# Kernel optimization log

Hardware: AMD Instinct MI355X
Metric: run time of the kernel (lower is better)

## Reference

```python
import jax, jax.numpy as jnp
import numpy as np

S = 4  # spixel_downsize


def _shift2d(x, oy, ox):
    # out[..., y, x] = x[..., y - oy, x - ox] if in-bounds else 0 (zero pad)
    pad = [(0, 0)] * (x.ndim - 2) + [(S, S), (S, S)]
    xp = jnp.pad(x, pad)
    h, w = x.shape[-2], x.shape[-1]
    return xp[..., S - oy:S - oy + h, S - ox:S - ox + w]


def _valid_mask(h, w, oy, ox):
    ys = jnp.arange(h)
    xs = jnp.arange(w)
    my = (ys - oy >= 0) & (ys - oy < h)
    mx = (xs - ox >= 0) & (xs - ox < w)
    return my[:, None] & mx[None, :]


def _conv3d(x, w, stride, pad):
    return jax.lax.conv_general_dilated(
        x, w, window_strides=stride, padding=[(p, p) for p in pad],
        dimension_numbers=('NCDHW', 'OIDHW', 'NCDHW'))


def _basic(x, w, stride, pad):
    # BasicConv: Conv3d(bias=False) + BN(identity at init) + ReLU
    return jax.nn.relu(_conv3d(x, w, stride, pad))


def setup_inputs() -> dict:
    key = jax.random.key(0)
    ks = jax.random.split(key, 8)
    cv = jax.random.normal(ks[0], (1, 8, 24, 128, 256), jnp.float32)
    sp = jax.random.uniform(ks[1], (1, 9, 128, 256), jnp.float32)
    xy = jax.random.normal(ks[2], (1, 2, 128, 256), jnp.float32)
    w_stem = jax.random.normal(ks[3], (16, 72, 1, 1, 1), jnp.float32) * 0.05
    w1a = jax.random.normal(ks[4], (32, 16, 3, 2, 2), jnp.float32) * 0.05
    w1b = jax.random.normal(ks[5], (32, 32, 3, 1, 1), jnp.float32) * 0.05
    w2a = jax.random.normal(ks[6], (64, 32, 3, 2, 2), jnp.float32) * 0.05
    w2b = jax.random.normal(ks[7], (64, 64, 3, 1, 1), jnp.float32) * 0.05
    return dict(cv=cv, sp=sp, xy=xy, w_stem=w_stem, w1a=w1a, w1b=w1b, w2a=w2a, w2b=w2b)


def reference(cv, sp, xy, w_stem, w1a, w1b, w2a, w2b):
    b, c, d, h, w = cv.shape
    feats, probs = [], []
    uv0 = jnp.zeros((b, 2, h, w), cv.dtype)
    # 9 shifted neighbors; neighbor k shifts by (S*((k//3)-1), S*((k%3)-1)).
    # All uv writes in the original target slot 0 and sequentially overwrite;
    for k in range(9):
        oy = S * ((k // 3) - 1)
        ox = S * ((k % 3) - 1)
        p = _shift2d(sp[:, k], oy, ox)                      # (b,h,w), zeros outside
        probs.append(p)
        feats.append(_shift2d(cv, oy, ox) * p[:, None, None])  # (b,c,d,h,w)
        u = _shift2d(xy, oy, ox) * p[:, None]               # (b,2,h,w)
        mask = _valid_mask(h, w, oy, ox)[None, None]
        uv0 = jnp.where(mask, u, uv0)
    # (b, c, 9, d, h, w) -> (b, 9c, d, h, w), matching torch reshape order
    feat = jnp.stack(feats, axis=2).reshape(b, c * 9, d, h, w)
    prob_sum = jnp.sum(jnp.stack(probs, axis=1), axis=1, keepdims=True)  # (b,1,h,w)
    tot = prob_sum.reshape(b, 1, h // S, S, w // S, S).mean((3, 5))      # avg_pool2d
    tot_up = jnp.repeat(jnp.repeat(tot, S, axis=2), S, axis=3)           # nearest upsample
    feat = feat / tot_up[:, :, None]                                     # (b,9c,d,h,w)
    feat = _basic(feat, w_stem, (1, 1, 1), (0, 0, 0))
    f1 = _basic(feat, w1a, (2, 2, 2), (1, 0, 0))
    f1 = _basic(f1, w1b, (1, 1, 1), (1, 0, 0))
    f2 = _basic(f1, w2a, (2, 2, 2), (1, 0, 0))
    f2 = _basic(f2, w2b, (1, 1, 1), (1, 0, 0))
    # uv.sum(2) == uv0 since only neighbor-slot 0 is written
    uv = uv0.reshape(b, 2, h // S, S, w // S, S).mean((3, 5)) / tot      # (b,2,h/S,w/S)
    return f1, f2, uv.reshape(b, 2, -1)
```

## Files before the change

### kernel.cpp

```cpp
#include <hip/hip_runtime.h>

#define HH 128
#define WW 256
#define HW (HH * WW)

#define OFF_TOT   0
#define OFF_WT    2048
#define WT_STEM   0
#define WT_1A     1152
#define WT_1B     7296
#define WT_2A     10368
#define WT_2B     34944
#define OFF_STEM  49280
#define OFF_F1A   12632192
#define OFF_F1N   15777920
#define OFF_F2A   49280

__global__ __launch_bounds__(256) void k_pre(
    const float* __restrict__ sp, const float* __restrict__ xy,
    const float* __restrict__ wstem, const float* __restrict__ w1a,
    const float* __restrict__ w1b, const float* __restrict__ w2a,
    const float* __restrict__ w2b,
    float* __restrict__ tot, float* __restrict__ uv_out, float* __restrict__ wt)
{
  int gid = blockIdx.x * 256 + threadIdx.x;
  if (gid < 1152) { int o = gid & 15, r = gid >> 4; int ci = r / 9, k = r - ci * 9;
    wt[WT_STEM + gid] = wstem[o * 72 + ci * 9 + k]; }
  if (gid < 6144) { int o = gid & 31, ci = (gid >> 5) & 15, tp = gid >> 9;
    wt[WT_1A + gid] = w1a[o * 192 + ci * 12 + tp]; }
  if (gid < 3072) { int o = gid & 31, ci = (gid >> 5) & 31, kd = gid >> 10;
    wt[WT_1B + gid] = w1b[(o * 32 + ci) * 3 + kd]; }
  if (gid < 24576) { int o = gid & 63, ci = (gid >> 6) & 31, tp = gid >> 11;
    wt[WT_2A + gid] = w2a[o * 384 + ci * 12 + tp]; }
  if (gid < 12288) { int o = gid & 63, ci = (gid >> 6) & 63, kd = gid >> 12;
    wt[WT_2B + gid] = w2b[(o * 64 + ci) * 3 + kd]; }
  if (gid < 8192) {
    int cell = gid >> 2, q = gid & 3;
    int Y = cell >> 6, X = cell & 63;
    float tsum = 0.f, u0 = 0.f, u1 = 0.f;
    int y = Y * 4 + q;
#pragma unroll
    for (int j = 0; j < 4; ++j) {
      int x = X * 4 + j;
      float psum = 0.f;
#pragma unroll
      for (int k = 0; k < 9; ++k) {
        int oy = 4 * ((k / 3) - 1), ox = 4 * ((k % 3) - 1);
        int sy = y - oy, sx = x - ox;
        if (sy >= 0 && sy < HH && sx >= 0 && sx < WW)
          psum += sp[k * HW + sy * WW + sx];
      }
      tsum += psum;
      int oy = (y >= 4) ? 4 : 0;
      int ox = (x >= 4) ? 4 : 0;
      int kk = (oy ? 2 : 1) * 3 + (ox ? 2 : 1);
      int sy = y - oy, sx = x - ox;
      float p = sp[kk * HW + sy * WW + sx];
      u0 += xy[sy * WW + sx] * p;
      u1 += xy[HW + sy * WW + sx] * p;
    }
    tsum += __shfl_xor(tsum, 1); tsum += __shfl_xor(tsum, 2);
    u0 += __shfl_xor(u0, 1); u0 += __shfl_xor(u0, 2);
    u1 += __shfl_xor(u1, 1); u1 += __shfl_xor(u1, 2);
    if (q == 0) {
      float t = tsum * (1.f / 16.f);
      tot[cell] = t;
      float inv = 1.f / t;
      uv_out[cell] = u0 * (1.f / 16.f) * inv;
      uv_out[2048 + cell] = u1 * (1.f / 16.f) * inv;
    }
  }
}

__global__ __launch_bounds__(256) void k_stem(
    const float* __restrict__ cv, const float* __restrict__ sp,
    const float* __restrict__ wt, const float* __restrict__ tot,
    float* __restrict__ out)
{
  __shared__ float wl[1152];
  for (int i = threadIdx.x; i < 1152; i += 256) wl[i] = wt[i];
  __syncthreads();
  int x0 = blockIdx.x * 128 + 2 * (threadIdx.x & 63);
  int y  = blockIdx.y * 4 + (threadIdx.x >> 6);
  int d  = blockIdx.z;
  float2 p2[9]; int off[9];
#pragma unroll
  for (int k = 0; k < 9; ++k) {
    int oy = 4 * ((k / 3) - 1), ox = 4 * ((k % 3) - 1);
    int sy = y - oy, sx = x0 - ox;
    bool v = (sy >= 0) && (sy < HH) && (sx >= 0) && (sx < WW - 1);
    int syc = v ? sy : 0, sxc = v ? sx : 0;
    off[k] = syc * WW + sxc;
    float2 t = *(const float2*)(sp + k * HW + off[k]);
    p2[k].x = v ? t.x : 0.f;
    p2[k].y = v ? t.y : 0.f;
  }
  float acc[16][2];
#pragma unroll
  for (int o = 0; o < 16; ++o) { acc[o][0] = 0.f; acc[o][1] = 0.f; }
  const float* cvd = cv + (size_t)d * HW;
  float2 cb[2][9];
#pragma unroll
  for (int k = 0; k < 9; ++k) cb[0][k] = *(const float2*)(cvd + off[k]);
#pragma unroll
  for (int ci = 0; ci < 8; ++ci) {
    if (ci < 7) {
#pragma unroll
      for (int k = 0; k < 9; ++k)
        cb[(ci + 1) & 1][k] = *(const float2*)(cvd + (size_t)(ci + 1) * 24 * HW + off[k]);
    }
#pragma unroll
    for (int k = 0; k < 9; ++k) {
      float t0 = cb[ci & 1][k].x * p2[k].x;
      float t1 = cb[ci & 1][k].y * p2[k].y;
      const float* wb = &wl[(ci * 9 + k) * 16];
      float wv[16];
#pragma unroll
      for (int q = 0; q < 4; ++q) *(float4*)&wv[q * 4] = *(const float4*)(wb + q * 4);
#pragma unroll
      for (int o = 0; o < 16; ++o) {
        acc[o][0] += wv[o] * t0;
        acc[o][1] += wv[o] * t1;
      }
    }
  }
  float inv = 1.f / tot[(y >> 2) * 64 + (x0 >> 2)];
  float* op = out + (((size_t)d * HH + y) * WW + x0) * 16;
#pragma unroll
  for (int p = 0; p < 2; ++p)
#pragma unroll
    for (int q = 0; q < 4; ++q) {
      float4 v;
      v.x = fmaxf(acc[q * 4 + 0][p] * inv, 0.f);
      v.y = fmaxf(acc[q * 4 + 1][p] * inv, 0.f);
      v.z = fmaxf(acc[q * 4 + 2][p] * inv, 0.f);
      v.w = fmaxf(acc[q * 4 + 3][p] * inv, 0.f);
      *(float4*)(op + p * 16 + q * 4) = v;
    }
}

__global__ __launch_bounds__(256) void k_conv1a(
    const float* __restrict__ in, const float* __restrict__ wt,
    float* __restrict__ out)
{
  __shared__ float wl[1536];
  int og = blockIdx.z;
  for (int i = threadIdx.x; i < 1536; i += 256) {
    int o = i & 7, ci = (i >> 3) & 15, tap = i >> 7;
    wl[i] = wt[tap * 512 + ci * 32 + og * 8 + o];
  }
  __syncthreads();
  int xo = threadIdx.x & 127;
  int yo = blockIdx.x * 2 + (threadIdx.x >> 7);
  int dz = blockIdx.y;
  float acc[8];
#pragma unroll
  for (int o = 0; o < 8; ++o) acc[o] = 0.f;
  float ib[2][32];
  {
    int dd = 2 * dz - 1; dd = dd < 0 ? 0 : dd;
    const float4* ip = (const float4*)(in + (((size_t)dd * 128 + 2 * yo) * 256 + 2 * xo) * 16);
#pragma unroll
    for (int q = 0; q < 8; ++q) {
      float4 t = ip[q];
      ib[0][q * 4] = t.x; ib[0][q * 4 + 1] = t.y; ib[0][q * 4 + 2] = t.z; ib[0][q * 4 + 3] = t.w;
    }
  }
#pragma unroll
  for (int w = 0; w < 6; ++w) {
    if (w < 5) {
      int kd = (w + 1) >> 1, ky = (w + 1) & 1;
      int dd = 2 * dz - 1 + kd; dd = dd < 0 ? 0 : dd;
      int y = 2 * yo + ky;
      const float4* ip = (const float4*)(in + (((size_t)dd * 128 + y) * 256 + 2 * xo) * 16);
#pragma unroll
      for (int q = 0; q < 8; ++q) {
        float4 t = ip[q];
        ib[(w + 1) & 1][q * 4] = t.x; ib[(w + 1) & 1][q * 4 + 1] = t.y;
        ib[(w + 1) & 1][q * 4 + 2] = t.z; ib[(w + 1) & 1][q * 4 + 3] = t.w;
      }
    }
    if (2 * dz - 1 + (w >> 1) >= 0) {
#pragma unroll
      for (int kx = 0; kx < 2; ++kx) {
        const float* wsl = &wl[(w * 2 + kx) * 128];
#pragma unroll
        for (int ci = 0; ci < 16; ++ci) {
          float wv[8];
          *(float4*)&wv[0] = *(const float4*)(wsl + ci * 8);
          *(float4*)&wv[4] = *(const float4*)(wsl + ci * 8 + 4);
          float a = ib[w & 1][kx * 16 + ci];
#pragma unroll
          for (int o = 0; o < 8; ++o) acc[o] += wv[o] * a;
        }
      }
    }
  }
  float* op = out + (((size_t)dz * 64 + yo) * 128 + xo) * 32 + og * 8;
  float4 v0, v1;
  v0.x = fmaxf(acc[0], 0.f); v0.y = fmaxf(acc[1], 0.f);
  v0.z = fmaxf(acc[2], 0.f); v0.w = fmaxf(acc[3], 0.f);
  v1.x = fmaxf(acc[4], 0.f); v1.y = fmaxf(acc[5], 0.f);
  v1.z = fmaxf(acc[6], 0.f); v1.w = fmaxf(acc[7], 0.f);
  *(float4*)op = v0; *(float4*)(op + 4) = v1;
}

__global__ __launch_bounds__(256) void k_conv1b(
    const float* __restrict__ in, const float* __restrict__ wt,
    float* __restrict__ outn, float* __restrict__ outc)
{
  __shared__ float wl[768];
  int og = blockIdx.z;
  for (int i = threadIdx.x; i < 768; i += 256) {
    int o = i & 7, ci = (i >> 3) & 31, kd = i >> 8;
    wl[i] = wt[kd * 1024 + ci * 32 + og * 8 + o];
  }
  __syncthreads();
  int xo = threadIdx.x & 127;
  int yo = blockIdx.x * 2 + (threadIdx.x >> 7);
  int dz = blockIdx.y;
  float acc[8];
#pragma unroll
  for (int o = 0; o < 8; ++o) acc[o] = 0.f;
  float ib[2][32];
  {
    int dd = dz - 1; dd = dd < 0 ? 0 : dd;
    const float4* ip = (const float4*)(in + (((size_t)dd * 64 + yo) * 128 + xo) * 32);
#pragma unroll
    for (int q = 0; q < 8; ++q) {
      float4 t = ip[q];
      ib[0][q * 4] = t.x; ib[0][q * 4 + 1] = t.y; ib[0][q * 4 + 2] = t.z; ib[0][q * 4 + 3] = t.w;
    }
  }
#pragma unroll
  for (int w = 0; w < 3; ++w) {
    if (w < 2) {
      int dd = dz + w;  dd = dd >= 12 ? 11 : dd;
      const float4* ip = (const float4*)(in + (((size_t)dd * 64 + yo) * 128 + xo) * 32);
#pragma unroll
      for (int q = 0; q < 8; ++q) {
        float4 t = ip[q];
        ib[(w + 1) & 1][q * 4] = t.x; ib[(w + 1) & 1][q * 4 + 1] = t.y;
        ib[(w + 1) & 1][q * 4 + 2] = t.z; ib[(w + 1) & 1][q * 4 + 3] = t.w;
      }
    }
    int d_ = dz - 1 + w;
    if (d_ >= 0 && d_ < 12) {
      const float* wsl = &wl[w * 256];
#pragma unroll
      for (int ci = 0; ci < 32; ++ci) {
        float wv[8];
        *(float4*)&wv[0] = *(const float4*)(wsl + ci * 8);
        *(float4*)&wv[4] = *(const float4*)(wsl + ci * 8 + 4);
        float a = ib[w & 1][ci];
#pragma unroll
        for (int o = 0; o < 8; ++o) acc[o] += wv[o] * a;
      }
    }
  }
  float* onp = outn + (((size_t)dz * 64 + yo) * 128 + xo) * 32 + og * 8;
  float4 v0, v1;
  v0.x = fmaxf(acc[0], 0.f); v0.y = fmaxf(acc[1], 0.f);
  v0.z = fmaxf(acc[2], 0.f); v0.w = fmaxf(acc[3], 0.f);
  v1.x = fmaxf(acc[4], 0.f); v1.y = fmaxf(acc[5], 0.f);
  v1.z = fmaxf(acc[6], 0.f); v1.w = fmaxf(acc[7], 0.f);
  *(float4*)onp = v0; *(float4*)(onp + 4) = v1;
#pragma unroll
  for (int o = 0; o < 8; ++o)
    outc[((size_t)((og * 8 + o) * 12 + dz) * 64 + yo) * 128 + xo] = fmaxf(acc[o], 0.f);
}

__global__ __launch_bounds__(256) void k_conv2a(
    const float* __restrict__ in, const float* __restrict__ wt,
    float* __restrict__ out)
{
  __shared__ float wl[1536];
  int og = blockIdx.z;
  for (int i = threadIdx.x; i < 1536; i += 256) {
    int o = i & 3, ci = (i >> 2) & 31, tap = i >> 7;
    wl[i] = wt[tap * 2048 + ci * 64 + og * 4 + o];
  }
  __syncthreads();
  int xo = threadIdx.x & 63;
  int yo = blockIdx.x * 4 + (threadIdx.x >> 6);
  int dz = blockIdx.y;
  float acc[4] = {0.f, 0.f, 0.f, 0.f};
  float ib[2][32];
  {
    int dd = 2 * dz - 1; dd = dd < 0 ? 0 : dd;
    const float4* ip = (const float4*)(in + (((size_t)dd * 64 + 2 * yo) * 128 + 2 * xo) * 32);
#pragma unroll
    for (int q = 0; q < 8; ++q) {
      float4 t = ip[q];
      ib[0][q * 4] = t.x; ib[0][q * 4 + 1] = t.y; ib[0][q * 4 + 2] = t.z; ib[0][q * 4 + 3] = t.w;
    }
  }
#pragma unroll
  for (int w = 0; w < 12; ++w) {
    if (w < 11) {
      int wn = w + 1;
      int kd = wn >> 2, ky = (wn >> 1) & 1, kx = wn & 1;
      int dd = 2 * dz - 1 + kd; dd = dd < 0 ? 0 : dd;
      int y = 2 * yo + ky, x = 2 * xo + kx;
      const float4* ip = (const float4*)(in + (((size_t)dd * 64 + y) * 128 + x) * 32);
#pragma unroll
      for (int q = 0; q < 8; ++q) {
        float4 t = ip[q];
        ib[wn & 1][q * 4] = t.x; ib[wn & 1][q * 4 + 1] = t.y;
        ib[wn & 1][q * 4 + 2] = t.z; ib[wn & 1][q * 4 + 3] = t.w;
      }
    }
    if (2 * dz - 1 + (w >> 2) >= 0) {
      const float* wsl = &wl[w * 128];
#pragma unroll
      for (int ci = 0; ci < 32; ++ci) {
        float wv[4];
        *(float4*)&wv[0] = *(const float4*)(wsl + ci * 4);
        float a = ib[w & 1][ci];
#pragma unroll
        for (int o = 0; o < 4; ++o) acc[o] += wv[o] * a;
      }
    }
  }
  float4 v;
  v.x = fmaxf(acc[0], 0.f); v.y = fmaxf(acc[1], 0.f);
  v.z = fmaxf(acc[2], 0.f); v.w = fmaxf(acc[3], 0.f);
  *(float4*)(out + (((size_t)dz * 32 + yo) * 64 + xo) * 64 + og * 4) = v;
}

__global__ __launch_bounds__(256) void k_conv2b(
    const float* __restrict__ in, const float* __restrict__ wt,
    float* __restrict__ out)
{
  __shared__ float wl[768];
  int og = blockIdx.z;
  for (int i = threadIdx.x; i < 768; i += 256) {
    int o = i & 3, ci = (i >> 2) & 63, kd = i >> 8;
    wl[i] = wt[kd * 4096 + ci * 64 + og * 4 + o];
  }
  __syncthreads();
  int xo = threadIdx.x & 63;
  int yo = blockIdx.x * 4 + (threadIdx.x >> 6);
  int dz = blockIdx.y;
  float acc[4] = {0.f, 0.f, 0.f, 0.f};
  float ib[2][32];
  {
    int dd = dz - 1; dd = dd < 0 ? 0 : dd;
    const float4* ip = (const float4*)(in + (((size_t)dd * 32 + yo) * 64 + xo) * 64);
#pragma unroll
    for (int q = 0; q < 8; ++q) {
      float4 t = ip[q];
      ib[0][q * 4] = t.x; ib[0][q * 4 + 1] = t.y; ib[0][q * 4 + 2] = t.z; ib[0][q * 4 + 3] = t.w;
    }
  }
#pragma unroll
  for (int w = 0; w < 6; ++w) {
    if (w < 5) {
      int wn = w + 1;
      int kd = wn >> 1, hf = wn & 1;
      int dd = dz - 1 + kd; dd = dd < 0 ? 0 : (dd >= 6 ? 5 : dd);
      const float4* ip = (const float4*)(in + (((size_t)dd * 32 + yo) * 64 + xo) * 64 + hf * 32);
#pragma unroll
      for (int q = 0; q < 8; ++q) {
        float4 t = ip[q];
        ib[wn & 1][q * 4] = t.x; ib[wn & 1][q * 4 + 1] = t.y;
        ib[wn & 1][q * 4 + 2] = t.z; ib[wn & 1][q * 4 + 3] = t.w;
      }
    }
    int d_ = dz - 1 + (w >> 1);
    if (d_ >= 0 && d_ < 6) {
      const float* wsl = &wl[w * 128];
#pragma unroll
      for (int ci = 0; ci < 32; ++ci) {
        float wv[4];
        *(float4*)&wv[0] = *(const float4*)(wsl + ci * 4);
        float a = ib[w & 1][ci];
#pragma unroll
        for (int o = 0; o < 4; ++o) acc[o] += wv[o] * a;
      }
    }
  }
#pragma unroll
  for (int o = 0; o < 4; ++o)
    out[((size_t)((og * 4 + o) * 6 + dz) * 32 + yo) * 64 + xo] = fmaxf(acc[o], 0.f);
}

extern "C" void kernel_launch(void* const* d_in, const int* in_sizes, int n_in,
                              void* d_out, int out_size, void* d_ws, size_t ws_size,
                              hipStream_t stream) {
  const float* cv    = (const float*)d_in[0];
  const float* sp    = (const float*)d_in[1];
  const float* xy    = (const float*)d_in[2];
  const float* wstem = (const float*)d_in[3];
  const float* w1a   = (const float*)d_in[4];
  const float* w1b   = (const float*)d_in[5];
  const float* w2a   = (const float*)d_in[6];
  const float* w2b   = (const float*)d_in[7];
  float* out = (float*)d_out;
  float* out_f1 = out;
  float* out_f2 = out + 3145728;
  float* out_uv = out + 3145728 + 786432;

  float* ws = (float*)d_ws;
  float* t_tot  = ws + OFF_TOT;
  float* wt     = ws + OFF_WT;
  float* t_stem = ws + OFF_STEM;
  float* t_f1a  = ws + OFF_F1A;
  float* t_f1n  = ws + OFF_F1N;
  float* t_f2a  = ws + OFF_F2A;

  k_pre<<<96, 256, 0, stream>>>(sp, xy, wstem, w1a, w1b, w2a, w2b,
                                t_tot, out_uv, wt);
  k_stem<<<dim3(2, 32, 24), 256, 0, stream>>>(cv, sp, wt + WT_STEM, t_tot, t_stem);
  k_conv1a<<<dim3(32, 12, 4), 256, 0, stream>>>(t_stem, wt + WT_1A, t_f1a);
  k_conv1b<<<dim3(32, 12, 4), 256, 0, stream>>>(t_f1a, wt + WT_1B, t_f1n, out_f1);
  k_conv2a<<<dim3(8, 6, 16), 256, 0, stream>>>(t_f1n, wt + WT_2A, t_f2a);
  k_conv2b<<<dim3(8, 6, 16), 256, 0, stream>>>(t_f2a, wt + WT_2B, out_f2);
}
```

Before: 181.6 us.

## Register-block conv kernels over 4 output pixels and use packed fp32 FMA

Each conv kernel (stem, conv1a, conv1b) now computes four adjacent output pixels per thread and splits output channels across blocks, so weights read from shared memory are reused across more pixels. Inner loops use two-wide vector FMA (v2f) so the compiler can emit packed fp32 FMA instructions. The input channel loop is chunked to keep register use bounded. In exchange, per-thread loads become strided across pixels, register pressure rises, and the stem now reads cv once per channel group, i.e. twice in total.

```diff
diff --git a/kernel.cpp b/kernel.cpp
--- a/kernel.cpp
+++ b/kernel.cpp
@@ -3,6 +3,16 @@
 #define HH 128
 #define WW 256
 #define HW (HH * WW)
+
+typedef float v2f __attribute__((ext_vector_type(2)));
+
+static __device__ __forceinline__ v2f fma2(v2f a, v2f b, v2f c) {
+#if __has_builtin(__builtin_elementwise_fma)
+  return __builtin_elementwise_fma(a, b, c);
+#else
+  return a * b + c;
+#endif
+}
 
 #define OFF_TOT   0
 #define OFF_WT    2048
@@ -77,66 +87,75 @@
     const float* __restrict__ wt, const float* __restrict__ tot,
     float* __restrict__ out)
 {
-  __shared__ float wl[1152];
-  for (int i = threadIdx.x; i < 1152; i += 256) wl[i] = wt[i];
+  __shared__ float wl[576];
+  int og = blockIdx.x;
+  for (int i = threadIdx.x; i < 576; i += 256)
+    wl[i] = wt[(i >> 3) * 16 + og * 8 + (i & 7)];
   __syncthreads();
-  int x0 = blockIdx.x * 128 + 2 * (threadIdx.x & 63);
+  int x0 = 4 * (threadIdx.x & 63);
   int y  = blockIdx.y * 4 + (threadIdx.x >> 6);
   int d  = blockIdx.z;
-  float2 p2[9]; int off[9];
+  int off[9];
+  float4 p4[9];
 #pragma unroll
   for (int k = 0; k < 9; ++k) {
     int oy = 4 * ((k / 3) - 1), ox = 4 * ((k % 3) - 1);
     int sy = y - oy, sx = x0 - ox;
-    bool v = (sy >= 0) && (sy < HH) && (sx >= 0) && (sx < WW - 1);
+    bool v = (sy >= 0) && (sy < HH) && (sx >= 0) && (sx <= WW - 4);
     int syc = v ? sy : 0, sxc = v ? sx : 0;
     off[k] = syc * WW + sxc;
-    float2 t = *(const float2*)(sp + k * HW + off[k]);
-    p2[k].x = v ? t.x : 0.f;
-    p2[k].y = v ? t.y : 0.f;
-  }
-  float acc[16][2];
-#pragma unroll
-  for (int o = 0; o < 16; ++o) { acc[o][0] = 0.f; acc[o][1] = 0.f; }
+    float4 t = *(const float4*)(sp + k * HW + off[k]);
+    float4 z = {0.f, 0.f, 0.f, 0.f};
+    p4[k] = v ? t : z;
+  }
+  v2f acc[4][4];
+#pragma unroll
+  for (int a = 0; a < 4; ++a)
+#pragma unroll
+    for (int p = 0; p < 4; ++p) acc[a][p] = (v2f){0.f, 0.f};
   const float* cvd = cv + (size_t)d * HW;
-  float2 cb[2][9];
-#pragma unroll
-  for (int k = 0; k < 9; ++k) cb[0][k] = *(const float2*)(cvd + off[k]);
+  float4 c[2];
+  c[0] = *(const float4*)(cvd + off[0]);
 #pragma unroll
   for (int ci = 0; ci < 8; ++ci) {
-    if (ci < 7) {
-#pragma unroll
-      for (int k = 0; k < 9; ++k)
-        cb[(ci + 1) & 1][k] = *(const float2*)(cvd + (size_t)(ci + 1) * 24 * HW + off[k]);
-    }
 #pragma unroll
     for (int k = 0; k < 9; ++k) {
-      float t0 = cb[ci & 1][k].x * p2[k].x;
-      float t1 = cb[ci & 1][k].y * p2[k].y;
-      const float* wb = &wl[(ci * 9 + k) * 16];
-      float wv[16];
-#pragma unroll
-      for (int q = 0; q < 4; ++q) *(float4*)&wv[q * 4] = *(const float4*)(wb + q * 4);
-#pragma unroll
-      for (int o = 0; o < 16; ++o) {
-        acc[o][0] += wv[o] * t0;
-        acc[o][1] += wv[o] * t1;
-      }
+      int n = ci * 9 + k;
+      if (n < 71) {
+        int n1 = n + 1, ci1 = n1 / 9, k1 = n1 - ci1 * 9;
+        c[n1 & 1] = *(const float4*)(cvd + (size_t)ci1 * 24 * HW + off[k1]);
+      }
+      float4 cc = c[n & 1];
+      float4 pp = p4[k];
+      float t0 = cc.x * pp.x, t1 = cc.y * pp.y, t2 = cc.z * pp.z, t3 = cc.w * pp.w;
+      const float* wb = &wl[n * 8];
+      float4 wq0 = *(const float4*)wb;
+      float4 wq1 = *(const float4*)(wb + 4);
+      v2f w0 = {wq0.x, wq0.y}, w1 = {wq0.z, wq0.w};
+      v2f w2 = {wq1.x, wq1.y}, w3 = {wq1.z, wq1.w};
+      v2f s0 = {t0, t0}, s1 = {t1, t1}, s2 = {t2, t2}, s3 = {t3, t3};
+      acc[0][0] = fma2(w0, s0, acc[0][0]); acc[1][0] = fma2(w1, s0, acc[1][0]);
+      acc[2][0] = fma2(w2, s0, acc[2][0]); acc[3][0] = fma2(w3, s0, acc[3][0]);
+      acc[0][1] = fma2(w0, s1, acc[0][1]); acc[1][1] = fma2(w1, s1, acc[1][1]);
+      acc[2][1] = fma2(w2, s1, acc[2][1]); acc[3][1] = fma2(w3, s1, acc[3][1]);
+      acc[0][2] = fma2(w0, s2, acc[0][2]); acc[1][2] = fma2(w1, s2, acc[1][2]);
+      acc[2][2] = fma2(w2, s2, acc[2][2]); acc[3][2] = fma2(w3, s2, acc[3][2]);
+      acc[0][3] = fma2(w0, s3, acc[0][3]); acc[1][3] = fma2(w1, s3, acc[1][3]);
+      acc[2][3] = fma2(w2, s3, acc[2][3]); acc[3][3] = fma2(w3, s3, acc[3][3]);
     }
   }
   float inv = 1.f / tot[(y >> 2) * 64 + (x0 >> 2)];
-  float* op = out + (((size_t)d * HH + y) * WW + x0) * 16;
-#pragma unroll
-  for (int p = 0; p < 2; ++p)
-#pragma unroll
-    for (int q = 0; q < 4; ++q) {
-      float4 v;
-      v.x = fmaxf(acc[q * 4 + 0][p] * inv, 0.f);
-      v.y = fmaxf(acc[q * 4 + 1][p] * inv, 0.f);
-      v.z = fmaxf(acc[q * 4 + 2][p] * inv, 0.f);
-      v.w = fmaxf(acc[q * 4 + 3][p] * inv, 0.f);
-      *(float4*)(op + p * 16 + q * 4) = v;
-    }
+  float* op = out + (((size_t)d * HH + y) * WW + x0) * 16 + og * 8;
+#pragma unroll
+  for (int p = 0; p < 4; ++p) {
+    float4 v0, v1;
+    v0.x = fmaxf(acc[0][p].x * inv, 0.f); v0.y = fmaxf(acc[0][p].y * inv, 0.f);
+    v0.z = fmaxf(acc[1][p].x * inv, 0.f); v0.w = fmaxf(acc[1][p].y * inv, 0.f);
+    v1.x = fmaxf(acc[2][p].x * inv, 0.f); v1.y = fmaxf(acc[2][p].y * inv, 0.f);
+    v1.z = fmaxf(acc[3][p].x * inv, 0.f); v1.w = fmaxf(acc[3][p].y * inv, 0.f);
+    *(float4*)(op + p * 16) = v0;
+    *(float4*)(op + p * 16 + 4) = v1;
+  }
 }
 
 __global__ __launch_bounds__(256) void k_conv1a(
@@ -150,124 +169,164 @@
     wl[i] = wt[tap * 512 + ci * 32 + og * 8 + o];
   }
   __syncthreads();
-  int xo = threadIdx.x & 127;
-  int yo = blockIdx.x * 2 + (threadIdx.x >> 7);
+  int xq = threadIdx.x & 31;
+  int xo0 = 4 * xq;
+  int yo = blockIdx.x * 8 + (threadIdx.x >> 5);
   int dz = blockIdx.y;
-  float acc[8];
-#pragma unroll
-  for (int o = 0; o < 8; ++o) acc[o] = 0.f;
+  v2f acc[4][4];
+#pragma unroll
+  for (int a = 0; a < 4; ++a)
+#pragma unroll
+    for (int p = 0; p < 4; ++p) acc[a][p] = (v2f){0.f, 0.f};
   float ib[2][32];
   {
     int dd = 2 * dz - 1; dd = dd < 0 ? 0 : dd;
-    const float4* ip = (const float4*)(in + (((size_t)dd * 128 + 2 * yo) * 256 + 2 * xo) * 16);
-#pragma unroll
-    for (int q = 0; q < 8; ++q) {
-      float4 t = ip[q];
-      ib[0][q * 4] = t.x; ib[0][q * 4 + 1] = t.y; ib[0][q * 4 + 2] = t.z; ib[0][q * 4 + 3] = t.w;
-    }
-  }
-#pragma unroll
-  for (int w = 0; w < 6; ++w) {
-    if (w < 5) {
-      int kd = (w + 1) >> 1, ky = (w + 1) & 1;
-      int dd = 2 * dz - 1 + kd; dd = dd < 0 ? 0 : dd;
-      int y = 2 * yo + ky;
-      const float4* ip = (const float4*)(in + (((size_t)dd * 128 + y) * 256 + 2 * xo) * 16);
-#pragma unroll
-      for (int q = 0; q < 8; ++q) {
-        float4 t = ip[q];
-        ib[(w + 1) & 1][q * 4] = t.x; ib[(w + 1) & 1][q * 4 + 1] = t.y;
-        ib[(w + 1) & 1][q * 4 + 2] = t.z; ib[(w + 1) & 1][q * 4 + 3] = t.w;
-      }
-    }
-    if (2 * dz - 1 + (w >> 1) >= 0) {
+    const float* base = in + (((size_t)dd * 128 + 2 * yo) * 256 + 8 * xq) * 16;
+#pragma unroll
+    for (int i = 0; i < 8; ++i) {
+      float4 t = *(const float4*)(base + i * 16);
+      ib[0][i * 4] = t.x; ib[0][i * 4 + 1] = t.y; ib[0][i * 4 + 2] = t.z; ib[0][i * 4 + 3] = t.w;
+    }
+  }
+#pragma unroll
+  for (int m = 0; m < 24; ++m) {
+    int kd = m >> 3, ky = (m >> 2) & 1, c4 = m & 3;
+    if (m < 23) {
+      int mn = m + 1;
+      int nkd = mn >> 3, nky = (mn >> 2) & 1, nc4 = mn & 3;
+      int dd = 2 * dz - 1 + nkd; dd = dd < 0 ? 0 : dd;
+      int y = 2 * yo + nky;
+      const float* base = in + (((size_t)dd * 128 + y) * 256 + 8 * xq) * 16 + nc4 * 4;
+#pragma unroll
+      for (int i = 0; i < 8; ++i) {
+        float4 t = *(const float4*)(base + i * 16);
+        ib[mn & 1][i * 4] = t.x; ib[mn & 1][i * 4 + 1] = t.y;
+        ib[mn & 1][i * 4 + 2] = t.z; ib[mn & 1][i * 4 + 3] = t.w;
+      }
+    }
+    if (2 * dz - 1 + kd >= 0) {
 #pragma unroll
       for (int kx = 0; kx < 2; ++kx) {
-        const float* wsl = &wl[(w * 2 + kx) * 128];
-#pragma unroll
-        for (int ci = 0; ci < 16; ++ci) {
-          float wv[8];
-          *(float4*)&wv[0] = *(const float4*)(wsl + ci * 8);
-          *(float4*)&wv[4] = *(const float4*)(wsl + ci * 8 + 4);
-          float a = ib[w & 1][kx * 16 + ci];
-#pragma unroll
-          for (int o = 0; o < 8; ++o) acc[o] += wv[o] * a;
+        int tap = (kd * 2 + ky) * 2 + kx;
+#pragma unroll
+        for (int j = 0; j < 4; ++j) {
+          int ci = c4 * 4 + j;
+          const float* wb = &wl[tap * 128 + ci * 8];
+          float4 wq0 = *(const float4*)wb;
+          float4 wq1 = *(const float4*)(wb + 4);
+          v2f w0 = {wq0.x, wq0.y}, w1 = {wq0.z, wq0.w};
+          v2f w2 = {wq1.x, wq1.y}, w3 = {wq1.z, wq1.w};
+#pragma unroll
+          for (int px = 0; px < 4; ++px) {
+            float a = ib[m & 1][(2 * px + kx) * 4 + j];
+            v2f as = {a, a};
+            acc[0][px] = fma2(w0, as, acc[0][px]);
+            acc[1][px] = fma2(w1, as, acc[1][px]);
+            acc[2][px] = fma2(w2, as, acc[2][px]);
+            acc[3][px] = fma2(w3, as, acc[3][px]);
+          }
         }
       }
     }
   }
-  float* op = out + (((size_t)dz * 64 + yo) * 128 + xo) * 32 + og * 8;
-  float4 v0, v1;
-  v0.x = fmaxf(acc[0], 0.f); v0.y = fmaxf(acc[1], 0.f);
-  v0.z = fmaxf(acc[2], 0.f); v0.w = fmaxf(acc[3], 0.f);
-  v1.x = fmaxf(acc[4], 0.f); v1.y = fmaxf(acc[5], 0.f);
-  v1.z = fmaxf(acc[6], 0.f); v1.w = fmaxf(acc[7], 0.f);
-  *(float4*)op = v0; *(float4*)(op + 4) = v1;
+  float* op = out + (((size_t)dz * 64 + yo) * 128 + xo0) * 32 + og * 8;
+#pragma unroll
+  for (int px = 0; px < 4; ++px) {
+    float4 v0, v1;
+    v0.x = fmaxf(acc[0][px].x, 0.f); v0.y = fmaxf(acc[0][px].y, 0.f);
+    v0.z = fmaxf(acc[1][px].x, 0.f); v0.w = fmaxf(acc[1][px].y, 0.f);
+    v1.x = fmaxf(acc[2][px].x, 0.f); v1.y = fmaxf(acc[2][px].y, 0.f);
+    v1.z = fmaxf(acc[3][px].x, 0.f); v1.w = fmaxf(acc[3][px].y, 0.f);
+    *(float4*)(op + px * 32) = v0;
+    *(float4*)(op + px * 32 + 4) = v1;
+  }
 }
 
 __global__ __launch_bounds__(256) void k_conv1b(
     const float* __restrict__ in, const float* __restrict__ wt,
     float* __restrict__ outn, float* __restrict__ outc)
 {
-  __shared__ float wl[768];
+  __shared__ float wl[384];
   int og = blockIdx.z;
-  for (int i = threadIdx.x; i < 768; i += 256) {
-    int o = i & 7, ci = (i >> 3) & 31, kd = i >> 8;
-    wl[i] = wt[kd * 1024 + ci * 32 + og * 8 + o];
+  for (int i = threadIdx.x; i < 384; i += 256) {
+    int o = i & 3, ci = (i >> 2) & 31, kd = i >> 7;
+    wl[i] = wt[kd * 1024 + ci * 32 + og * 4 + o];
   }
   __syncthreads();
-  int xo = threadIdx.x & 127;
-  int yo = blockIdx.x * 2 + (threadIdx.x >> 7);
+  int xq = threadIdx.x & 31;
+  int xo0 = 4 * xq;
+  int yo = blockIdx.x * 8 + (threadIdx.x >> 5);
   int dz = blockIdx.y;
-  float acc[8];
-#pragma unroll
-  for (int o = 0; o < 8; ++o) acc[o] = 0.f;
+  v2f acc[2][4];
+#pragma unroll
+  for (int a = 0; a < 2; ++a)
+#pragma unroll
+    for (int p = 0; p < 4; ++p) acc[a][p] = (v2f){0.f, 0.f};
   float ib[2][32];
   {
     int dd = dz - 1; dd = dd < 0 ? 0 : dd;
-    const float4* ip = (const float4*)(in + (((size_t)dd * 64 + yo) * 128 + xo) * 32);
-#pragma unroll
-    for (int q = 0; q < 8; ++q) {
-      float4 t = ip[q];
-      ib[0][q * 4] = t.x; ib[0][q * 4 + 1] = t.y; ib[0][q * 4 + 2] = t.z; ib[0][q * 4 + 3] = t.w;
-    }
-  }
-#pragma unroll
-  for (int w = 0; w < 3; ++w) {
-    if (w < 2) {
-      int dd = dz + w;  dd = dd >= 12 ? 11 : dd;
-      const float4* ip = (const float4*)(in + (((size_t)dd * 64 + yo) * 128 + xo) * 32);
-#pragma unroll
-      for (int q = 0; q < 8; ++q) {
-        float4 t = ip[q];
-        ib[(w + 1) & 1][q * 4] = t.x; ib[(w + 1) & 1][q * 4 + 1] = t.y;
-        ib[(w + 1) & 1][q * 4 + 2] = t.z; ib[(w + 1) & 1][q * 4 + 3] = t.w;
-      }
-    }
-    int d_ = dz - 1 + w;
+    const float* base = in + (((size_t)dd * 64 + yo) * 128 + xo0) * 32;
+#pragma unroll
+    for (int i = 0; i < 4; ++i) {
+      float4 t0 = *(const float4*)(base + i * 32);
+      float4 t1 = *(const float4*)(base + i * 32 + 4);
+      ib[0][i * 8] = t0.x; ib[0][i * 8 + 1] = t0.y; ib[0][i * 8 + 2] = t0.z; ib[0][i * 8 + 3] = t0.w;
+      ib[0][i * 8 + 4] = t1.x; ib[0][i * 8 + 5] = t1.y; ib[0][i * 8 + 6] = t1.z; ib[0][i * 8 + 7] = t1.w;
+    }
+  }
+#pragma unroll
+  for (int m = 0; m < 12; ++m) {
+    int kd = m >> 2, ch = m & 3;
+    if (m < 11) {
+      int mn = m + 1;
+      int nkd = mn >> 2, nch = mn & 3;
+      int dd = dz - 1 + nkd; dd = dd < 0 ? 0 : (dd >= 12 ? 11 : dd);
+      const float* base = in + (((size_t)dd * 64 + yo) * 128 + xo0) * 32 + nch * 8;
+#pragma unroll
+      for (int i = 0; i < 4; ++i) {
+        float4 t0 = *(const float4*)(base + i * 32);
+        float4 t1 = *(const float4*)(base + i * 32 + 4);
+        ib[mn & 1][i * 8] = t0.x; ib[mn & 1][i * 8 + 1] = t0.y;
+        ib[mn & 1][i * 8 + 2] = t0.z; ib[mn & 1][i * 8 + 3] = t0.w;
+        ib[mn & 1][i * 8 + 4] = t1.x; ib[mn & 1][i * 8 + 5] = t1.y;
+        ib[mn & 1][i * 8 + 6] = t1.z; ib[mn & 1][i * 8 + 7] = t1.w;
+      }
+    }
+    int d_ = dz - 1 + kd;
     if (d_ >= 0 && d_ < 12) {
-      const float* wsl = &wl[w * 256];
-#pragma unroll
-      for (int ci = 0; ci < 32; ++ci) {
-        float wv[8];
-        *(float4*)&wv[0] = *(const float4*)(wsl + ci * 8);
-        *(float4*)&wv[4] = *(const float4*)(wsl + ci * 8 + 4);
-        float a = ib[w & 1][ci];
-#pragma unroll
-        for (int o = 0; o < 8; ++o) acc[o] += wv[o] * a;
-      }
-    }
-  }
-  float* onp = outn + (((size_t)dz * 64 + yo) * 128 + xo) * 32 + og * 8;
-  float4 v0, v1;
-  v0.x = fmaxf(acc[0], 0.f); v0.y = fmaxf(acc[1], 0.f);
-  v0.z = fmaxf(acc[2], 0.f); v0.w = fmaxf(acc[3], 0.f);
-  v1.x = fmaxf(acc[4], 0.f); v1.y = fmaxf(acc[5], 0.f);
-  v1.z = fmaxf(acc[6], 0.f); v1.w = fmaxf(acc[7], 0.f);
-  *(float4*)onp = v0; *(float4*)(onp + 4) = v1;
-#pragma unroll
-  for (int o = 0; o < 8; ++o)
-    outc[((size_t)((og * 8 + o) * 12 + dz) * 64 + yo) * 128 + xo] = fmaxf(acc[o], 0.f);
+#pragma unroll
+      for (int j = 0; j < 8; ++j) {
+        int ci = ch * 8 + j;
+        float4 wq = *(const float4*)&wl[kd * 128 + ci * 4];
+        v2f w0 = {wq.x, wq.y}, w1 = {wq.z, wq.w};
+#pragma unroll
+        for (int px = 0; px < 4; ++px) {
+          float a = ib[m & 1][px * 8 + j];
+          v2f as = {a, a};
+          acc[0][px] = fma2(w0, as, acc[0][px]);
+          acc[1][px] = fma2(w1, as, acc[1][px]);
+        }
+      }
+    }
+  }
+  float* onp = outn + (((size_t)dz * 64 + yo) * 128 + xo0) * 32 + og * 4;
+#pragma unroll
+  for (int px = 0; px < 4; ++px) {
+    float4 v;
+    v.x = fmaxf(acc[0][px].x, 0.f); v.y = fmaxf(acc[0][px].y, 0.f);
+    v.z = fmaxf(acc[1][px].x, 0.f); v.w = fmaxf(acc[1][px].y, 0.f);
+    *(float4*)(onp + px * 32) = v;
+  }
+#pragma unroll
+  for (int o = 0; o < 4; ++o) {
+    float4 v;
+    float a0 = (o & 1) ? acc[o >> 1][0].y : acc[o >> 1][0].x;
+    float a1 = (o & 1) ? acc[o >> 1][1].y : acc[o >> 1][1].x;
+    float a2 = (o & 1) ? acc[o >> 1][2].y : acc[o >> 1][2].x;
+    float a3 = (o & 1) ? acc[o >> 1][3].y : acc[o >> 1][3].x;
+    v.x = fmaxf(a0, 0.f); v.y = fmaxf(a1, 0.f); v.z = fmaxf(a2, 0.f); v.w = fmaxf(a3, 0.f);
+    *(float4*)(outc + (((size_t)(og * 4 + o) * 12 + dz) * 64 + yo) * 128 + xo0) = v;
+  }
 }
 
 __global__ __launch_bounds__(256) void k_conv2a(
@@ -284,7 +343,7 @@
   int xo = threadIdx.x & 63;
   int yo = blockIdx.x * 4 + (threadIdx.x >> 6);
   int dz = blockIdx.y;
-  float acc[4] = {0.f, 0.f, 0.f, 0.f};
+  v2f acc[2] = {{0.f, 0.f}, {0.f, 0.f}};
   float ib[2][32];
   {
     int dd = 2 * dz - 1; dd = dd < 0 ? 0 : dd;
@@ -314,17 +373,18 @@
       const float* wsl = &wl[w * 128];
 #pragma unroll
       for (int ci = 0; ci < 32; ++ci) {
-        float wv[4];
-        *(float4*)&wv[0] = *(const float4*)(wsl + ci * 4);
+        float4 wq = *(const float4*)(wsl + ci * 4);
+        v2f w0 = {wq.x, wq.y}, w1 = {wq.z, wq.w};
         float a = ib[w & 1][ci];
-#pragma unroll
-        for (int o = 0; o < 4; ++o) acc[o] += wv[o] * a;
+        v2f as = {a, a};
+        acc[0] = fma2(w0, as, acc[0]);
+        acc[1] = fma2(w1, as, acc[1]);
       }
     }
   }
   float4 v;
-  v.x = fmaxf(acc[0], 0.f); v.y = fmaxf(acc[1], 0.f);
-  v.z = fmaxf(acc[2], 0.f); v.w = fmaxf(acc[3], 0.f);
+  v.x = fmaxf(acc[0].x, 0.f); v.y = fmaxf(acc[0].y, 0.f);
+  v.z = fmaxf(acc[1].x, 0.f); v.w = fmaxf(acc[1].y, 0.f);
   *(float4*)(out + (((size_t)dz * 32 + yo) * 64 + xo) * 64 + og * 4) = v;
 }
 
@@ -342,7 +402,7 @@
   int xo = threadIdx.x & 63;
   int yo = blockIdx.x * 4 + (threadIdx.x >> 6);
   int dz = blockIdx.y;
-  float acc[4] = {0.f, 0.f, 0.f, 0.f};
+  v2f acc[2] = {{0.f, 0.f}, {0.f, 0.f}};
   float ib[2][32];
   {
     int dd = dz - 1; dd = dd < 0 ? 0 : dd;
@@ -369,20 +429,23 @@
     }
     int d_ = dz - 1 + (w >> 1);
     if (d_ >= 0 && d_ < 6) {
-      const float* wsl = &wl[w * 128];
+      const float* wsl = &wl[(w >> 1) * 256 + (w & 1) * 128];
 #pragma unroll
       for (int ci = 0; ci < 32; ++ci) {
-        float wv[4];
-        *(float4*)&wv[0] = *(const float4*)(wsl + ci * 4);
+        float4 wq = *(const float4*)(wsl + ci * 4);
+        v2f w0 = {wq.x, wq.y}, w1 = {wq.z, wq.w};
         float a = ib[w & 1][ci];
-#pragma unroll
-        for (int o = 0; o < 4; ++o) acc[o] += wv[o] * a;
-      }
-    }
-  }
-#pragma unroll
-  for (int o = 0; o < 4; ++o)
-    out[((size_t)((og * 4 + o) * 6 + dz) * 32 + yo) * 64 + xo] = fmaxf(acc[o], 0.f);
+        v2f as = {a, a};
+        acc[0] = fma2(w0, as, acc[0]);
+        acc[1] = fma2(w1, as, acc[1]);
+      }
+    }
+  }
+#pragma unroll
+  for (int o = 0; o < 4; ++o) {
+    float a = (o & 1) ? acc[o >> 1].y : acc[o >> 1].x;
+    out[((size_t)((og * 4 + o) * 6 + dz) * 32 + yo) * 64 + xo] = fmaxf(a, 0.f);
+  }
 }
 
 extern "C" void kernel_launch(void* const* d_in, const int* in_sizes, int n_in,
@@ -412,8 +475,8 @@
   k_pre<<<96, 256, 0, stream>>>(sp, xy, wstem, w1a, w1b, w2a, w2b,
                                 t_tot, out_uv, wt);
   k_stem<<<dim3(2, 32, 24), 256, 0, stream>>>(cv, sp, wt + WT_STEM, t_tot, t_stem);
-  k_conv1a<<<dim3(32, 12, 4), 256, 0, stream>>>(t_stem, wt + WT_1A, t_f1a);
-  k_conv1b<<<dim3(32, 12, 4), 256, 0, stream>>>(t_f1a, wt + WT_1B, t_f1n, out_f1);
+  k_conv1a<<<dim3(8, 12, 4), 256, 0, stream>>>(t_stem, wt + WT_1A, t_f1a);
+  k_conv1b<<<dim3(8, 12, 8), 256, 0, stream>>>(t_f1a, wt + WT_1B, t_f1n, out_f1);
   k_conv2a<<<dim3(8, 6, 16), 256, 0, stream>>>(t_f1n, wt + WT_2A, t_f2a);
   k_conv2b<<<dim3(8, 6, 16), 256, 0, stream>>>(t_f2a, wt + WT_2B, out_f2);
 }
```

After: 219.3 us. +20.7%, slower.
